# Kernel optimization log

Measured on AMD Instinct MI355X. Metric: run time of the kernel, lower is better.

The kernel has to match this reference:

```python
import jax, jax.numpy as jnp
import numpy as np

SQRT_DK = np.sqrt(512.0).astype(np.float32)


def setup_inputs() -> dict:
    key = jax.random.key(0)
    k1, k2, k3 = jax.random.split(key, 3)
    x = jax.random.normal(k1, (16, 2048, 512), dtype=jnp.float32)
    W1 = jax.random.normal(k2, (512, 10), dtype=jnp.float32) * 0.05
    W2 = jax.random.normal(k3, (10, 512), dtype=jnp.float32) * 0.05
    return {"x": x, "W1": W1, "W2": W2}


def reference(x, W1, W2):
    # x: [B, A, D]; low-rank bilinear scores: (x@W1) @ (W2@x^T) -> [B, A, A]
    B, A, D = x.shape
    left = jnp.einsum('bad,dr->bar', x, W1)          # [B, A, 10]
    right = jnp.einsum('rd,bcd->brc', W2, x)         # [B, 10, A]
    scores = jnp.einsum('bar,brc->bac', left, right)  # [B, A, A]
    attn = jax.nn.softmax(scores / SQRT_DK, axis=-1)
    out = jnp.einsum('bac,bcd->bad', attn, x)         # requires_value=True
    return out
```

## Files before the change

kernel.cpp:

```cpp
#include <hip/hip_runtime.h>
#include <cstdint>
#include <cstddef>


typedef float    f32x4 __attribute__((ext_vector_type(4)));
typedef _Float16 half8 __attribute__((ext_vector_type(8)));
typedef _Float16 half4 __attribute__((ext_vector_type(4)));
typedef _Float16 half2 __attribute__((ext_vector_type(2)));

#define B_  16
#define A_  2048
#define D_  512
#define KSCALE 0.06375872f

#define SCHED_FENCE() __builtin_amdgcn_sched_barrier(0)

__device__ inline float fast_exp2(float v) {
#if __has_builtin(__builtin_amdgcn_exp2f)
    return __builtin_amdgcn_exp2f(v);
#else
    return __expf(v * 0.6931471805599453f);
#endif
}

__global__ __launch_bounds__(256) void kw_prep(const float* __restrict__ W1,
                                               const float* __restrict__ W2,
                                               _Float16* __restrict__ Wf) {
    int pi = blockIdx.x * 256 + threadIdx.x;
    int kt = pi >> 6, lane = pi & 63;
    int quad = lane >> 4, col = lane & 15;
    half8 h1, h2;
#pragma unroll
    for (int j = 0; j < 8; ++j) {
        int d = kt * 32 + quad * 8 + j;
        h1[j] = (col < 10) ? (_Float16)(W1[d * 10 + col] * KSCALE) : (_Float16)0.f;
        h2[j] = (col < 10) ? (_Float16)W2[col * 512 + d] : (_Float16)0.f;
    }
    *(half8*)(Wf + (size_t)pi * 16) = h1;
    *(half8*)(Wf + (size_t)pi * 16 + 8) = h2;
}

__global__ __launch_bounds__(256) void k01_prep(const float* __restrict__ x,
                                                const _Float16* __restrict__ Wf,
                                                _Float16* __restrict__ xT,
                                                _Float16* __restrict__ left16,
                                                _Float16* __restrict__ rightT16) {
    __shared__ float xs[32 * 64];
    int t = threadIdx.x, lane = t & 63, w = t >> 6;
    int quad = lane >> 4, c16 = lane & 15;
    int bid = blockIdx.x;
    int b = bid >> 6, grp = bid & 63;
    int c0 = grp << 5;
    const float* xb = x + ((size_t)b * A_ + c0) * D_;
    int tile = w >> 1, kki = w & 1;
    int ar = tile * 16 + c16;
    f32x4 accA = {0.f, 0.f, 0.f, 0.f}, accB = {0.f, 0.f, 0.f, 0.f};

    for (int dc = 0; dc < 8; ++dc) {
        __syncthreads();
#pragma unroll
        for (int p = 0; p < 2; ++p) {
            int c = p * 16 + (t >> 4), ch = t & 15;
            float4 v = *(const float4*)(xb + (size_t)c * D_ + dc * 64 + ch * 4);
            *(float4*)&xs[c * 64 + ((ch ^ (c & 15)) << 2)] = v;
        }
        __syncthreads();
        {
            int dloc = t >> 2, c8 = (t & 3) << 3;
            int ch = dloc >> 2, e = dloc & 3;
            half8 h;
#pragma unroll
            for (int j = 0; j < 8; ++j) {
                int c = c8 + j;
                h[j] = (_Float16)xs[c * 64 + ((ch ^ (c & 15)) << 2) + e];
            }
            *(half8*)(xT + ((size_t)b * D_ + dc * 64 + dloc) * A_ + c0 + c8) = h;
        }
        {
            int kk = kki * 32;
            int ch0 = (kk >> 2) + quad * 2;
            float4 v0 = *(const float4*)&xs[ar * 64 + ((ch0 ^ c16) << 2)];
            float4 v1 = *(const float4*)&xs[ar * 64 + (((ch0 + 1) ^ c16) << 2)];
            half8 af;
            af[0] = (_Float16)v0.x; af[1] = (_Float16)v0.y; af[2] = (_Float16)v0.z; af[3] = (_Float16)v0.w;
            af[4] = (_Float16)v1.x; af[5] = (_Float16)v1.y; af[6] = (_Float16)v1.z; af[7] = (_Float16)v1.w;
            const half8* wf = (const half8*)(Wf + ((size_t)((dc * 2 + kki) * 64 + lane)) * 16);
            half8 b1 = wf[0], b2 = wf[1];
            accA = __builtin_amdgcn_mfma_f32_16x16x32_f16(af, b1, accA, 0, 0, 0);
            accB = __builtin_amdgcn_mfma_f32_16x16x32_f16(af, b2, accB, 0, 0, 0);
        }
    }
    __syncthreads();
    float* red = xs;
    if (kki == 0) {
#pragma unroll
        for (int q = 0; q < 4; ++q) {
            red[tile * 512 + (quad * 4 + q) * 16 + c16] = accA[q];
            red[tile * 512 + 256 + (quad * 4 + q) * 16 + c16] = accB[q];
        }
    }
    __syncthreads();
    if (kki == 1) {
#pragma unroll
        for (int q = 0; q < 4; ++q) {
            float a = accA[q] + red[tile * 512 + (quad * 4 + q) * 16 + c16];
            float bb = accB[q] + red[tile * 512 + 256 + (quad * 4 + q) * 16 + c16];
            size_t grow = (size_t)bid * 32 + tile * 16 + quad * 4 + q;
            left16[grow * 16 + c16] = (_Float16)a;
            rightT16[grow * 16 + c16] = (_Float16)bb;
        }
    }
}

__global__ __launch_bounds__(512, 4) void k3_attn(const _Float16* __restrict__ xT,
                                                  const _Float16* __restrict__ left16,
                                                  const _Float16* __restrict__ rightT16,
                                                  float* __restrict__ out) {
    __shared__ _Float16 XTl[2][256 * 32];
    __shared__ _Float16 Ps[2][128 * 40];
    __shared__ float rowsum[128];
    int t = threadIdx.x, lane = t & 63, w = t >> 6;
    int quad = lane >> 4, c16 = lane & 15;
    int bid = blockIdx.x;
    int combo = (bid & 7) | (((bid >> 7) & 3) << 3);
    int at = (bid >> 3) & 15;
    int b = combo >> 1, nb = combo & 1;
    int a0 = at << 7, n0 = nb << 8;
    int waveM = w & 1, waveN = w >> 1;

    half8 lf8 = (half8)(_Float16)0.f;
    if (quad < 2) {
        int arow = a0 + w * 16 + c16;
        lf8 = *(const half8*)(left16 + ((size_t)(b << 11) + arow) * 16 + quad * 8);
    }

    f32x4 acc[4][4];
#pragma unroll
    for (int mi = 0; mi < 4; ++mi)
#pragma unroll
        for (int ni = 0; ni < 4; ++ni) acc[mi][ni] = (f32x4){0.f, 0.f, 0.f, 0.f};
    float psum = 0.f;

    const _Float16* xTb = xT + ((size_t)b * D_ + n0) * A_;
    const _Float16* rTb = rightT16 + (size_t)(b << 11) * 16;

    int nloc0 = w * 32 + (lane >> 2);
    int kq = lane & 3;
    int psrow = (w * 16 + c16) * 40;

    auto dma_tile = [&](int kt, int buf) {
        int c0 = kt << 5;
#pragma unroll
        for (int cc = 0; cc < 2; ++cc) {
            int nl = nloc0 + cc * 16;
            int kqs = kq ^ ((nl >> 1) & 3);
            const _Float16* src = xTb + (size_t)nl * A_ + c0 + kqs * 8;
            _Float16* dst = &XTl[buf][(w * 32 + cc * 16) * 32];
            __builtin_amdgcn_global_load_lds((const __attribute__((address_space(1))) void*)src,
                                             (__attribute__((address_space(3))) void*)dst,
                                             16, 0, 0);
        }
    };
    auto load_bfr = [&](int kt, half8* bfr) {
#pragma unroll
        for (int nh = 0; nh < 2; ++nh) {
            bfr[nh] = (half8)(_Float16)0.f;
            if (quad < 2) {
                int crow = (kt << 5) + nh * 16 + c16;
                bfr[nh] = *(const half8*)(rTb + (size_t)crow * 16 + quad * 8);
            }
        }
    };

    half8 bfr_cur[2], bfr_nxt[2];
    load_bfr(0, bfr_cur);
    dma_tile(0, 0);
    {
        f32x4 zz = {0.f, 0.f, 0.f, 0.f};
        f32x4 p0 = __builtin_amdgcn_mfma_f32_16x16x32_f16(bfr_cur[0], lf8, zz, 0, 0, 0);
        f32x4 p1 = __builtin_amdgcn_mfma_f32_16x16x32_f16(bfr_cur[1], lf8, zz, 0, 0, 0);
        float e0 = fast_exp2(p0[0]), e1 = fast_exp2(p0[1]), e2 = fast_exp2(p0[2]), e3 = fast_exp2(p0[3]);
        float f0 = fast_exp2(p1[0]), f1 = fast_exp2(p1[1]), f2 = fast_exp2(p1[2]), f3 = fast_exp2(p1[3]);
        psum += (e0 + e1) + (e2 + e3) + (f0 + f1) + (f2 + f3);
        half4 pv0, pv1;
        pv0[0] = (_Float16)e0; pv0[1] = (_Float16)e1; pv0[2] = (_Float16)e2; pv0[3] = (_Float16)e3;
        pv1[0] = (_Float16)f0; pv1[1] = (_Float16)f1; pv1[2] = (_Float16)f2; pv1[3] = (_Float16)f3;
        *(half4*)&Ps[0][psrow + quad * 4] = pv0;
        *(half4*)&Ps[0][psrow + 16 + quad * 4] = pv1;
    }
    load_bfr(1, bfr_cur);

    for (int kt = 0; kt < 63; ++kt) {
        __syncthreads();
        int cb = kt & 1, nx = kt + 1;

        f32x4 zz = {0.f, 0.f, 0.f, 0.f};
        f32x4 pc0 = __builtin_amdgcn_mfma_f32_16x16x32_f16(bfr_cur[0], lf8, zz, 0, 0, 0);
        f32x4 pc1 = __builtin_amdgcn_mfma_f32_16x16x32_f16(bfr_cur[1], lf8, zz, 0, 0, 0);
        dma_tile(nx, nx & 1);
        {
            int ktn = (kt + 2 < 64) ? kt + 2 : 0;
            load_bfr(ktn, bfr_nxt);
        }
        half8 bf[4];
#pragma unroll
        for (int ni = 0; ni < 4; ++ni) {
            int nr = waveN * 64 + ni * 16 + c16;
            bf[ni] = *(const half8*)&XTl[cb][nr * 32 + ((quad ^ ((nr >> 1) & 3)) << 3)];
        }
        half8 af0 = *(const half8*)&Ps[cb][(waveM * 64 + c16) * 40 + quad * 8];
        SCHED_FENCE();

        half8 af1 = *(const half8*)&Ps[cb][(waveM * 64 + 16 + c16) * 40 + quad * 8];
#pragma unroll
        for (int ni = 0; ni < 4; ++ni)
            acc[0][ni] = __builtin_amdgcn_mfma_f32_16x16x32_f16(af0, bf[ni], acc[0][ni], 0, 0, 0);
        float e0 = fast_exp2(pc0[0]), e1 = fast_exp2(pc0[1]);
        float e2 = fast_exp2(pc0[2]), e3 = fast_exp2(pc0[3]);
        psum += (e0 + e1) + (e2 + e3);
        half4 pv0;
        pv0[0] = (_Float16)e0; pv0[1] = (_Float16)e1; pv0[2] = (_Float16)e2; pv0[3] = (_Float16)e3;
        SCHED_FENCE();

        half8 af2 = *(const half8*)&Ps[cb][(waveM * 64 + 32 + c16) * 40 + quad * 8];
#pragma unroll
        for (int ni = 0; ni < 4; ++ni)
            acc[1][ni] = __builtin_amdgcn_mfma_f32_16x16x32_f16(af1, bf[ni], acc[1][ni], 0, 0, 0);
        float f0 = fast_exp2(pc1[0]), f1 = fast_exp2(pc1[1]);
        float f2 = fast_exp2(pc1[2]), f3 = fast_exp2(pc1[3]);
        psum += (f0 + f1) + (f2 + f3);
        half4 pv1;
        pv1[0] = (_Float16)f0; pv1[1] = (_Float16)f1; pv1[2] = (_Float16)f2; pv1[3] = (_Float16)f3;
        SCHED_FENCE();

        half8 af3 = *(const half8*)&Ps[cb][(waveM * 64 + 48 + c16) * 40 + quad * 8];
#pragma unroll
        for (int ni = 0; ni < 4; ++ni)
            acc[2][ni] = __builtin_amdgcn_mfma_f32_16x16x32_f16(af2, bf[ni], acc[2][ni], 0, 0, 0);
        *(half4*)&Ps[nx & 1][psrow + quad * 4] = pv0;
        SCHED_FENCE();

#pragma unroll
        for (int ni = 0; ni < 4; ++ni)
            acc[3][ni] = __builtin_amdgcn_mfma_f32_16x16x32_f16(af3, bf[ni], acc[3][ni], 0, 0, 0);
        *(half4*)&Ps[nx & 1][psrow + 16 + quad * 4] = pv1;
        bfr_cur[0] = bfr_nxt[0];
        bfr_cur[1] = bfr_nxt[1];
    }

    __syncthreads();
    {
        const int cb = 1;
        half8 bf[4];
#pragma unroll
        for (int ni = 0; ni < 4; ++ni) {
            int nr = waveN * 64 + ni * 16 + c16;
            bf[ni] = *(const half8*)&XTl[cb][nr * 32 + ((quad ^ ((nr >> 1) & 3)) << 3)];
        }
#pragma unroll
        for (int mi = 0; mi < 4; ++mi) {
            half8 af = *(const half8*)&Ps[cb][(waveM * 64 + mi * 16 + c16) * 40 + quad * 8];
#pragma unroll
            for (int ni = 0; ni < 4; ++ni)
                acc[mi][ni] = __builtin_amdgcn_mfma_f32_16x16x32_f16(af, bf[ni], acc[mi][ni], 0, 0, 0);
        }
    }

    {
        float s = psum;
        s += __shfl_xor(s, 16);
        s += __shfl_xor(s, 32);
        if (quad == 0) rowsum[w * 16 + c16] = s;
    }
    __syncthreads();

    float* ob = out + ((size_t)b * A_ + a0) * D_ + n0;
#pragma unroll
    for (int mi = 0; mi < 4; ++mi) {
#pragma unroll
        for (int q = 0; q < 4; ++q) {
            int ar = waveM * 64 + mi * 16 + quad * 4 + q;
            float sc = 1.0f / rowsum[ar];
#pragma unroll
            for (int ni = 0; ni < 4; ++ni)
                ob[(size_t)ar * D_ + waveN * 64 + ni * 16 + c16] = acc[mi][ni][q] * sc;
        }
    }
}

extern "C" void kernel_launch(void* const* d_in, const int* in_sizes, int n_in,
                              void* d_out, int out_size, void* d_ws, size_t ws_size,
                              hipStream_t stream) {
    const float* x  = (const float*)d_in[0];
    const float* W1 = (const float*)d_in[1];
    const float* W2 = (const float*)d_in[2];
    float* out = (float*)d_out;
    char* ws = (char*)d_ws;
    _Float16* xT      = (_Float16*)ws;
    _Float16* left16  = (_Float16*)(ws + 33554432);
    _Float16* rightT16= (_Float16*)(ws + 34603008);
    _Float16* Wf      = (_Float16*)(ws + 35651584);

    kw_prep<<<4, 256, 0, stream>>>(W1, W2, Wf);
    k01_prep<<<1024, 256, 0, stream>>>(x, Wf, xT, left16, rightT16);
    k3_attn<<<512, 512, 0, stream>>>(xT, left16, rightT16, out);
}
```

Baseline: 206.3 us.

## Fuse weight packing into prep kernel and prefetch next x chunk into registers

Removes the separate kw_prep launch; each k01_prep thread now builds its own fp16 W1/W2 fragments directly from the fp32 weights on the fly. The global load of the next x chunk is also issued right after the barrier, so it overlaps with the current chunk's transpose and MFMA work. This saves one kernel launch and hides some load latency. In exchange, every block repeats the strided scalar weight loads and conversions, and register use goes up.

Measured after the change: 210.1 us. About the same (+1.8%).

```diff
diff --git a/kernel.cpp b/kernel.cpp
--- a/kernel.cpp
+++ b/kernel.cpp
@@ -6,7 +6,6 @@
 typedef float    f32x4 __attribute__((ext_vector_type(4)));
 typedef _Float16 half8 __attribute__((ext_vector_type(8)));
 typedef _Float16 half4 __attribute__((ext_vector_type(4)));
-typedef _Float16 half2 __attribute__((ext_vector_type(2)));
 
 #define B_  16
 #define A_  2048
@@ -23,25 +22,9 @@
 #endif
 }
 
-__global__ __launch_bounds__(256) void kw_prep(const float* __restrict__ W1,
-                                               const float* __restrict__ W2,
-                                               _Float16* __restrict__ Wf) {
-    int pi = blockIdx.x * 256 + threadIdx.x;
-    int kt = pi >> 6, lane = pi & 63;
-    int quad = lane >> 4, col = lane & 15;
-    half8 h1, h2;
-#pragma unroll
-    for (int j = 0; j < 8; ++j) {
-        int d = kt * 32 + quad * 8 + j;
-        h1[j] = (col < 10) ? (_Float16)(W1[d * 10 + col] * KSCALE) : (_Float16)0.f;
-        h2[j] = (col < 10) ? (_Float16)W2[col * 512 + d] : (_Float16)0.f;
-    }
-    *(half8*)(Wf + (size_t)pi * 16) = h1;
-    *(half8*)(Wf + (size_t)pi * 16 + 8) = h2;
-}
-
 __global__ __launch_bounds__(256) void k01_prep(const float* __restrict__ x,
-                                                const _Float16* __restrict__ Wf,
+                                                const float* __restrict__ W1,
+                                                const float* __restrict__ W2,
                                                 _Float16* __restrict__ xT,
                                                 _Float16* __restrict__ left16,
                                                 _Float16* __restrict__ rightT16) {
@@ -54,25 +37,48 @@
     const float* xb = x + ((size_t)b * A_ + c0) * D_;
     int tile = w >> 1, kki = w & 1;
     int ar = tile * 16 + c16;
+    int col = c16;
     f32x4 accA = {0.f, 0.f, 0.f, 0.f}, accB = {0.f, 0.f, 0.f, 0.f};
+
+    int cA = (t >> 4), cB = 16 + (t >> 4), ch = t & 15;
+    const float* srcA = xb + (size_t)cA * D_ + ch * 4;
+    const float* srcB = xb + (size_t)cB * D_ + ch * 4;
+    int dstA = cA * 64 + ((ch ^ (cA & 15)) << 2);
+    int dstB = cB * 64 + ((ch ^ (cB & 15)) << 2);
+
+    auto wf_make = [&](int kt, half8& h1, half8& h2) {
+        int dbase = kt * 32 + quad * 8;
+#pragma unroll
+        for (int j = 0; j < 8; ++j) {
+            int d = dbase + j;
+            h1[j] = (col < 10) ? (_Float16)(W1[d * 10 + col] * KSCALE) : (_Float16)0.f;
+            h2[j] = (col < 10) ? (_Float16)W2[col * 512 + d] : (_Float16)0.f;
+        }
+    };
+
+    float4 rA = *(const float4*)(srcA);
+    float4 rB = *(const float4*)(srcB);
+    half8 wf1c, wf2c, wf1n, wf2n;
+    wf_make(kki, wf1c, wf2c);
 
     for (int dc = 0; dc < 8; ++dc) {
         __syncthreads();
-#pragma unroll
-        for (int p = 0; p < 2; ++p) {
-            int c = p * 16 + (t >> 4), ch = t & 15;
-            float4 v = *(const float4*)(xb + (size_t)c * D_ + dc * 64 + ch * 4);
-            *(float4*)&xs[c * 64 + ((ch ^ (c & 15)) << 2)] = v;
-        }
+        *(float4*)&xs[dstA] = rA;
+        *(float4*)&xs[dstB] = rB;
         __syncthreads();
+        if (dc < 7) {
+            rA = *(const float4*)(srcA + (dc + 1) * 64);
+            rB = *(const float4*)(srcB + (dc + 1) * 64);
+        }
+        SCHED_FENCE();
         {
             int dloc = t >> 2, c8 = (t & 3) << 3;
-            int ch = dloc >> 2, e = dloc & 3;
+            int chh = dloc >> 2, e = dloc & 3;
             half8 h;
 #pragma unroll
             for (int j = 0; j < 8; ++j) {
                 int c = c8 + j;
-                h[j] = (_Float16)xs[c * 64 + ((ch ^ (c & 15)) << 2) + e];
+                h[j] = (_Float16)xs[c * 64 + ((chh ^ (c & 15)) << 2) + e];
             }
             *(half8*)(xT + ((size_t)b * D_ + dc * 64 + dloc) * A_ + c0 + c8) = h;
         }
@@ -84,10 +90,12 @@
             half8 af;
             af[0] = (_Float16)v0.x; af[1] = (_Float16)v0.y; af[2] = (_Float16)v0.z; af[3] = (_Float16)v0.w;
             af[4] = (_Float16)v1.x; af[5] = (_Float16)v1.y; af[6] = (_Float16)v1.z; af[7] = (_Float16)v1.w;
-            const half8* wf = (const half8*)(Wf + ((size_t)((dc * 2 + kki) * 64 + lane)) * 16);
-            half8 b1 = wf[0], b2 = wf[1];
-            accA = __builtin_amdgcn_mfma_f32_16x16x32_f16(af, b1, accA, 0, 0, 0);
-            accB = __builtin_amdgcn_mfma_f32_16x16x32_f16(af, b2, accB, 0, 0, 0);
+            accA = __builtin_amdgcn_mfma_f32_16x16x32_f16(af, wf1c, accA, 0, 0, 0);
+            accB = __builtin_amdgcn_mfma_f32_16x16x32_f16(af, wf2c, accB, 0, 0, 0);
+        }
+        if (dc < 7) {
+            wf_make((dc + 1) * 2 + kki, wf1n, wf2n);
+            wf1c = wf1n; wf2c = wf2n;
         }
     }
     __syncthreads();
@@ -299,9 +307,7 @@
     _Float16* xT      = (_Float16*)ws;
     _Float16* left16  = (_Float16*)(ws + 33554432);
     _Float16* rightT16= (_Float16*)(ws + 34603008);
-    _Float16* Wf      = (_Float16*)(ws + 35651584);
-
-    kw_prep<<<4, 256, 0, stream>>>(W1, W2, Wf);
-    k01_prep<<<1024, 256, 0, stream>>>(x, Wf, xT, left16, rightT16);
+
+    k01_prep<<<1024, 256, 0, stream>>>(x, W1, W2, xT, left16, rightT16);
     k3_attn<<<512, 512, 0, stream>>>(xT, left16, rightT16, out);
 }
```
